# Kernel tuning notes

Measured on AMD Instinct MI355X. Metric: run time of the kernel, lower is better.

The kernel has to match this reference:

```python
import jax, jax.numpy as jnp
import numpy as np

D_MODEL = 128; D_STATE = 64; D_CONV = 4; EXPAND = 2; HEADDIM = 32; NGROUPS = 1
D_INNER = EXPAND * D_MODEL            # 256
NHEADS = D_INNER // HEADDIM           # 8
CONV_DIM = D_INNER + 2 * NGROUPS * D_STATE   # 384 (x, B, C streams)
D_IN_PROJ = 2 * D_INNER + 2 * NGROUPS * D_STATE + NHEADS  # 648 (z, xBC, dt)
EPS = 1e-5


def setup_inputs() -> dict:
    key = jax.random.key(0)
    ks = jax.random.split(key, 8)
    B, L = 8, 4096
    x = jax.random.normal(ks[0], (B, L, D_MODEL), jnp.float32)
    norm_w = jnp.ones((D_MODEL,), jnp.float32)
    in_proj_w = jax.random.normal(ks[1], (D_IN_PROJ, D_MODEL), jnp.float32) * (D_MODEL ** -0.5)
    conv_w = jax.random.normal(ks[2], (CONV_DIM, D_CONV), jnp.float32) * (D_CONV ** -0.5)
    conv_b = jnp.zeros((CONV_DIM,), jnp.float32)
    dt_bias = jax.random.uniform(ks[3], (NHEADS,), jnp.float32, -4.0, -1.0)
    A_log = jnp.log(jax.random.uniform(ks[4], (NHEADS,), jnp.float32, 1.0, 16.0))
    D = jnp.ones((NHEADS,), jnp.float32)
    gnorm_w = jnp.ones((D_INNER,), jnp.float32)
    out_proj_w = jax.random.normal(ks[5], (D_MODEL, D_INNER), jnp.float32) * (D_INNER ** -0.5)
    return dict(x=x, norm_w=norm_w, in_proj_w=in_proj_w, conv_w=conv_w, conv_b=conv_b,
                dt_bias=dt_bias, A_log=A_log, D=D, gnorm_w=gnorm_w, out_proj_w=out_proj_w)


def _rmsnorm(x, w):
    return x * jax.lax.rsqrt(jnp.mean(x * x, axis=-1, keepdims=True) + EPS) * w


def _causal_dw_conv(x, w, b):
    # x: [B,L,C]; w: [C,K]; depthwise causal conv along L
    K = w.shape[1]
    xp = jnp.pad(x, ((0, 0), (K - 1, 0), (0, 0)))
    kern = jnp.transpose(w)[:, None, :]  # [K,1,C] for WIO with groups=C
    out = jax.lax.conv_general_dilated(
        xp, kern, window_strides=(1,), padding='VALID',
        dimension_numbers=('NWC', 'WIO', 'NWC'),
        feature_group_count=w.shape[0])
    return out + b


def _ssm(xh, dt, Bm, Cm, A):
    # xh: [B,L,H,P]; dt: [B,L,H]; Bm, Cm: [B,L,N]; A: [H]
    def step(h, inp):
        x_t, dt_t, B_t, C_t = inp
        dA = jnp.exp(dt_t * A)                                   # [B,H]
        h = h * dA[..., None, None] + (dt_t[..., None] * x_t)[..., None] * B_t[:, None, None, :]
        y = jnp.einsum('bhpn,bn->bhp', h, C_t)
        return h, y
    Bsz, L, H, P = xh.shape
    N = Bm.shape[-1]
    h0 = jnp.zeros((Bsz, H, P, N), xh.dtype)
    xs = (xh.transpose(1, 0, 2, 3), dt.transpose(1, 0, 2),
          Bm.transpose(1, 0, 2), Cm.transpose(1, 0, 2))
    _, ys = jax.lax.scan(step, h0, xs)
    return ys.transpose(1, 0, 2, 3)  # [B,L,H,P]


def reference(x, norm_w, in_proj_w, conv_w, conv_b, dt_bias, A_log, D, gnorm_w, out_proj_w):
    xn = _rmsnorm(x, norm_w)
    zxbcdt = xn @ in_proj_w.T                                    # [B,L,648]
    z, xBC, dt = jnp.split(zxbcdt, [D_INNER, D_INNER + CONV_DIM], axis=-1)
    dt = jax.nn.softplus(dt + dt_bias)                           # [B,L,H]
    xBC = jax.nn.silu(_causal_dw_conv(xBC, conv_w, conv_b))
    xs, Bm, Cm = jnp.split(xBC, [D_INNER, D_INNER + NGROUPS * D_STATE], axis=-1)
    Bsz, L, _ = x.shape
    xh = xs.reshape(Bsz, L, NHEADS, HEADDIM)
    A = -jnp.exp(A_log)                                          # [H]
    y = _ssm(xh, dt, Bm, Cm, A) + D[None, None, :, None] * xh    # D skip per head
    y = y.reshape(Bsz, L, D_INNER)
    y = _rmsnorm(y * jax.nn.silu(z), gnorm_w)                    # gated RMSNorm
    out = y @ out_proj_w.T
    return x + out
```

## Files before the change

### kernel.cpp

```cpp
#include <hip/hip_runtime.h>

#define DM    128
#define DI    256
#define NH    8
#define HD    32
#define NS    64
#define CDIM  384
#define DPROJ 648
#define LSEQ  4096
#define NB    8
#define NTOK  32768
#define LC    64
#define NC    64
#define EPSF  1e-5f
#define LOG2E 1.4426950408889634f

typedef __bf16 bf16;
typedef bf16  bf16x8 __attribute__((ext_vector_type(8)));
typedef bf16  bf16x4 __attribute__((ext_vector_type(4)));
typedef short short8 __attribute__((ext_vector_type(8)));
typedef float f32x4  __attribute__((ext_vector_type(4)));

__device__ __forceinline__ unsigned short f2bfbits(float f) {
    unsigned int u = __float_as_uint(f);
    unsigned int r = u + 0x7FFFu + ((u >> 16) & 1u);
    return (unsigned short)(r >> 16);
}
__device__ __forceinline__ float bfbits2f(unsigned short u) {
    return __uint_as_float(((unsigned int)u) << 16);
}

__global__ __launch_bounds__(256) void k_prep(const float* __restrict__ w1,
                                              const float* __restrict__ w2,
                                              const float* __restrict__ gw,
                                              unsigned short* __restrict__ w1g,
                                              unsigned short* __restrict__ w2f) {
    int i = blockIdx.x * 256 + threadIdx.x;
    if (i < 640 * DM) {
        int f = i >> 9, r = i & 511;
        int lane = r >> 3, jj = r & 7;
        int ns = f >> 2, kk = f & 3;
        int n = ns * 16 + (lane & 15), k = kk * 32 + (lane >> 4) * 8 + jj;
        w1g[i] = f2bfbits(w1[(size_t)n * DM + k]);
    } else {
        int j = i - 640 * DM;
        if (j < DM * DI) {
            int f = j >> 9, r = j & 511;
            int lane = r >> 3, jj = r & 7;
            int kk = f >> 3, nt = f & 7;
            int fr = lane & 15, ko = lane >> 4;
            int n = nt * 16 + fr, k = kk * 32 + ko * 8 + jj;
            w2f[j] = f2bfbits(w2[(size_t)n * DI + k] * gw[k]);
        }
    }
}

__global__ __launch_bounds__(256, 4) void k_gemm1(const float* __restrict__ x,
                                                  const float* __restrict__ nw,
                                                  const float* __restrict__ w1,
                                                  const float* __restrict__ dtb,
                                                  const unsigned short* __restrict__ w1g,
                                                  unsigned short* __restrict__ zb,
                                                  unsigned short* __restrict__ xbc,
                                                  float* __restrict__ dtf) {
    __shared__ float Xs[64][132];
    __shared__ float Wd[8][132];
    const int t = threadIdx.x;
    const int wave = t >> 6, lane = t & 63;
    const int m0 = blockIdx.x * 64;
    const int ny = blockIdx.y;
    if (ny == 0) {
        int row = t >> 5, col = (t & 31) * 4;
        *(float4*)&Wd[row][col] = *(const float4*)(w1 + (size_t)(640 + row) * DM + col);
    }
    const float nw0 = nw[lane * 2], nw1 = nw[lane * 2 + 1];
    #pragma unroll
    for (int i = 0; i < 16; i++) {
        int r = wave * 16 + i;
        const float* xr = x + (size_t)(m0 + r) * DM + lane * 2;
        float v0 = xr[0], v1 = xr[1];
        float ss = v0 * v0 + v1 * v1;
        #pragma unroll
        for (int o = 32; o; o >>= 1) ss += __shfl_xor(ss, o);
        float rs = rsqrtf(ss * (1.0f / DM) + EPSF);
        Xs[r][lane * 2]     = v0 * rs * nw0;
        Xs[r][lane * 2 + 1] = v1 * rs * nw1;
    }
    __syncthreads();
    if (ny == 0) {
        const int h = lane >> 3, ks = lane & 7;
        const float dtbh = dtb[h];
        #pragma unroll
        for (int i = 0; i < 16; i++) {
            int r = wave * 16 + i;
            float acc = 0.f;
            #pragma unroll
            for (int q = 0; q < 4; q++) {
                float4 xv = *(const float4*)&Xs[r][ks * 16 + q * 4];
                float4 wv = *(const float4*)&Wd[h][ks * 16 + q * 4];
                acc = fmaf(xv.x, wv.x, acc); acc = fmaf(xv.y, wv.y, acc);
                acc = fmaf(xv.z, wv.z, acc); acc = fmaf(xv.w, wv.w, acc);
            }
            acc += __shfl_xor(acc, 1);
            acc += __shfl_xor(acc, 2);
            acc += __shfl_xor(acc, 4);
            if (ks == 0) {
                float v = acc + dtbh;
                dtf[(size_t)(m0 + r) * NH + h] = (v > 20.f) ? v : log1pf(expf(v));
            }
        }
    }
    const int wm = wave >> 1, wn = wave & 1;
    const int fr = lane & 15, ko = lane >> 4;
    bf16x8 a[2][4];
    #pragma unroll
    for (int mt = 0; mt < 2; mt++)
        #pragma unroll
        for (int kk = 0; kk < 4; kk++) {
            const float* src = &Xs[wm * 32 + mt * 16 + fr][kk * 32 + ko * 8];
            float4 lo = *(const float4*)src, hi = *(const float4*)(src + 4);
            bf16x8 af;
            af[0] = (bf16)lo.x; af[1] = (bf16)lo.y; af[2] = (bf16)lo.z; af[3] = (bf16)lo.w;
            af[4] = (bf16)hi.x; af[5] = (bf16)hi.y; af[6] = (bf16)hi.z; af[7] = (bf16)hi.w;
            a[mt][kk] = af;
        }
    for (int i = 0; i < 5; i++) {
        int nt = ny * 5 + i;
        const unsigned short* wb = w1g + (((size_t)(nt * 4 + wn * 2) * 4) << 9) + lane * 8;
        f32x4 acc[2][2] = {};
        #pragma unroll
        for (int kk = 0; kk < 4; kk++) {
            bf16x8 b0 = *(const bf16x8*)(wb + ((size_t)kk << 9));
            bf16x8 b1 = *(const bf16x8*)(wb + ((size_t)(4 + kk) << 9));
            acc[0][0] = __builtin_amdgcn_mfma_f32_16x16x32_bf16(a[0][kk], b0, acc[0][0], 0, 0, 0);
            acc[1][0] = __builtin_amdgcn_mfma_f32_16x16x32_bf16(a[1][kk], b0, acc[1][0], 0, 0, 0);
            acc[0][1] = __builtin_amdgcn_mfma_f32_16x16x32_bf16(a[0][kk], b1, acc[0][1], 0, 0, 0);
            acc[1][1] = __builtin_amdgcn_mfma_f32_16x16x32_bf16(a[1][kk], b1, acc[1][1], 0, 0, 0);
        }
        unsigned short* dst; int ld, nc0;
        if (nt < 4) { dst = zb;  ld = DI;   nc0 = nt * 64; }
        else        { dst = xbc; ld = CDIM; nc0 = nt * 64 - 256; }
        #pragma unroll
        for (int mt = 0; mt < 2; mt++)
            #pragma unroll
            for (int ntt = 0; ntt < 2; ntt++) {
                int n = nc0 + wn * 32 + ntt * 16 + fr;
                #pragma unroll
                for (int rr = 0; rr < 4; rr++) {
                    int m = m0 + wm * 32 + mt * 16 + ko * 4 + rr;
                    dst[(size_t)m * ld + n] = f2bfbits(acc[mt][ntt][rr]);
                }
            }
    }
}

__global__ __launch_bounds__(512) void k_conv1(const unsigned short* __restrict__ xbc,
                                               const float* __restrict__ cw,
                                               const float* __restrict__ cb,
                                               const float* __restrict__ dtf,
                                               const float* __restrict__ alog,
                                               unsigned short* __restrict__ bcA,
                                               unsigned short* __restrict__ xT,
                                               unsigned short* __restrict__ hst,
                                               float* __restrict__ dAp) {
    __shared__ __align__(16) unsigned short L[320][72];
    __shared__ float wlh[NH][64];
    const int tid = threadIdx.x;
    const int t0 = blockIdx.x * 64;
    if (tid < CDIM) {
        const int ch = tid;
        const int l0 = t0 & (LSEQ - 1);
        float4 wv = *(const float4*)(cw + ch * 4);
        float bias = cb[ch];
        const unsigned short* in = xbc + (size_t)t0 * CDIM + ch;
        float h1 = 0.f, h2 = 0.f, h3 = 0.f;
        if (l0) {
            h1 = bfbits2f(in[-CDIM]);
            h2 = bfbits2f(in[-2 * CDIM]);
            h3 = bfbits2f(in[-3 * CDIM]);
        }
        short8 pk;
        #pragma unroll 8
        for (int t = 0; t < 64; t++) {
            float x0 = bfbits2f(in[(size_t)t * CDIM]);
            float acc = bias;
            acc = fmaf(x0, wv.w, acc);
            acc = fmaf(h1, wv.z, acc);
            acc = fmaf(h2, wv.y, acc);
            acc = fmaf(h3, wv.x, acc);
            float s = acc / (1.f + expf(-acc));
            unsigned short us = f2bfbits(s);
            if (ch >= 256) bcA[(size_t)(t0 + t) * 128 + (ch - 256)] = us;
            pk[t & 7] = (short)us;
            if (ch < 320 && (t & 7) == 7) *(short8*)&L[ch][t - 7] = pk;
            h3 = h2; h2 = h1; h1 = x0;
        }
    }
    __syncthreads();
    {
        int idx = tid;
        #pragma unroll
        for (int it = 0; it < 4; it++, idx += 512) {
            int row = idx >> 3, tc = (idx & 7) * 8;
            *(short8*)(xT + (size_t)row * NTOK + t0 + tc) = *(const short8*)&L[row][tc];
        }
    }
    const int h = tid >> 6, lane = tid & 63;
    const int b = blockIdx.x >> 6, c = blockIdx.x & 63;
    const int bh = b * NH + h;
    const float A = -expf(alog[h]);
    float dt = dtf[(size_t)(t0 + lane) * NH + h];
    float q = dt * A * LOG2E;
    #pragma unroll
    for (int o = 1; o <= 32; o <<= 1) {
        float tmp = __shfl_up(q, o);
        if (lane >= o) q += tmp;
    }
    float qL = __shfl(q, 63);
    wlh[h][lane] = exp2f(qL - q) * dt;
    if (lane == 0) dAp[(size_t)bh * NC + c] = exp2f(qL);
    const int m = lane & 15, ko = lane >> 4;
    f32x4 hacc[4][2] = {};
    #pragma unroll
    for (int kh = 0; kh < 2; kh++) {
        bf16x8 xb[2];
        #pragma unroll
        for (int pi = 0; pi < 2; pi++)
            xb[pi] = *(const bf16x8*)&L[h * HD + pi * 16 + m][kh * 32 + ko * 8];
        f32x4 w0 = *(const f32x4*)&wlh[h][kh * 32 + ko * 8];
        f32x4 w1v = *(const f32x4*)&wlh[h][kh * 32 + ko * 8 + 4];
        #pragma unroll
        for (int ni = 0; ni < 4; ni++) {
            bf16x8 bv = *(const bf16x8*)&L[256 + ni * 16 + m][kh * 32 + ko * 8];
            bf16x8 af;
            #pragma unroll
            for (int j = 0; j < 4; j++) af[j] = (bf16)((float)bv[j] * w0[j]);
            #pragma unroll
            for (int j = 0; j < 4; j++) af[4 + j] = (bf16)((float)bv[4 + j] * w1v[j]);
            #pragma unroll
            for (int pi = 0; pi < 2; pi++)
                hacc[ni][pi] = __builtin_amdgcn_mfma_f32_16x16x32_bf16(af, xb[pi], hacc[ni][pi], 0, 0, 0);
        }
    }
    unsigned short* hb = hst + (((size_t)bh * NC + c) << 11);
    #pragma unroll
    for (int ni = 0; ni < 4; ni++)
        #pragma unroll
        for (int pi = 0; pi < 2; pi++) {
            bf16x4 pv;
            #pragma unroll
            for (int r = 0; r < 4; r++) pv[r] = (bf16)hacc[ni][pi][r];
            *(bf16x4*)(hb + (pi * 16 + m) * 64 + ni * 16 + ko * 4) = pv;
        }
}

__global__ __launch_bounds__(256) void k_ssm2(unsigned short* __restrict__ hst,
                                              const float* __restrict__ dAp) {
    __shared__ float dl[NC];
    const int bh = blockIdx.x >> 3, seg = blockIdx.x & 7;
    const int s = seg * 256 + threadIdx.x;
    if (threadIdx.x < NC) dl[threadIdx.x] = dAp[(size_t)bh * NC + threadIdx.x];
    __syncthreads();
    unsigned short* p = hst + ((size_t)bh * NC << 11) + s;
    float r = 0.f;
    float v0 = bfbits2f(p[0]);
    float v1 = bfbits2f(p[(size_t)1 << 11]);
    float v2 = bfbits2f(p[(size_t)2 << 11]);
    float v3 = bfbits2f(p[(size_t)3 << 11]);
    for (int c = 0; c < NC; c += 4) {
        float t;
        t = v0; if (c + 4 < NC) v0 = bfbits2f(p[(size_t)(c + 4) << 11]);
        p[(size_t)c << 11] = f2bfbits(r);       r = fmaf(r, dl[c], t);
        t = v1; if (c + 5 < NC) v1 = bfbits2f(p[(size_t)(c + 5) << 11]);
        p[(size_t)(c + 1) << 11] = f2bfbits(r); r = fmaf(r, dl[c + 1], t);
        t = v2; if (c + 6 < NC) v2 = bfbits2f(p[(size_t)(c + 6) << 11]);
        p[(size_t)(c + 2) << 11] = f2bfbits(r); r = fmaf(r, dl[c + 2], t);
        t = v3; if (c + 7 < NC) v3 = bfbits2f(p[(size_t)(c + 7) << 11]);
        p[(size_t)(c + 3) << 11] = f2bfbits(r); r = fmaf(r, dl[c + 3], t);
    }
}

__global__ __launch_bounds__(512, 2) void k_ssd3g(const unsigned short* __restrict__ bcA,
                                                  const unsigned short* __restrict__ xT,
                                                  const float* __restrict__ dtf,
                                                  const float* __restrict__ alog,
                                                  const unsigned short* __restrict__ hst,
                                                  const float* __restrict__ Dw,
                                                  const unsigned short* __restrict__ zb,
                                                  const unsigned short* __restrict__ w2f,
                                                  const float* __restrict__ xin,
                                                  float* __restrict__ out) {
    __shared__ __align__(16) unsigned short BC[64][136];
    __shared__ __align__(16) bf16 PlY[NH][64 * 40];
    __shared__ float ql[NH][64];
    __shared__ float dl[NH][64];
    const int tid = threadIdx.x;
    const int b = blockIdx.x >> 6, c = blockIdx.x & 63;
    const int t0 = blockIdx.x * 64;
    const size_t tok0 = (size_t)t0;
    {
        int idx = tid;
        #pragma unroll
        for (int it = 0; it < 2; it++, idx += 512) {
            int tok = idx >> 4, c8 = (idx & 15) * 8;
            *(short8*)&BC[tok][c8] = *(const short8*)(bcA + (tok0 + tok) * 128 + c8);
        }
    }
    __syncthreads();
    const int h = tid >> 6, lane = tid & 63;
    const int bh = b * NH + h;
    const float A = -expf(alog[h]);
    const float Dh = Dw[h];
    float dt = dtf[(tok0 + lane) * NH + h];
    float q = dt * A * LOG2E;
    #pragma unroll
    for (int o = 1; o <= 32; o <<= 1) {
        float tmp = __shfl_up(q, o);
        if (lane >= o) q += tmp;
    }
    ql[h][lane] = q;
    dl[h][lane] = dt;
    const int m = lane & 15, ko = lane >> 4;
    bf16* Pw = &PlY[h][0];
    bf16x8 cf[4][2];
    #pragma unroll
    for (int ti = 0; ti < 4; ti++)
        #pragma unroll
        for (int kh = 0; kh < 2; kh++)
            cf[ti][kh] = *(const bf16x8*)&BC[ti * 16 + m][64 + kh * 32 + ko * 8];
    float qt[4];
    #pragma unroll
    for (int ti = 0; ti < 4; ti++) qt[ti] = ql[h][ti * 16 + m];
    const size_t hbase = ((size_t)bh * NC + c) << 11;
    f32x4 ya[4][2] = {}, ua[4][2] = {};
    #pragma unroll
    for (int kh = 0; kh < 2; kh++) {
        bf16x8 hb2[2];
        #pragma unroll
        for (int pi = 0; pi < 2; pi++)
            hb2[pi] = *(const bf16x8*)(hst + hbase + (pi * 16 + m) * 64 + kh * 32 + ko * 8);
        #pragma unroll
        for (int ti = 0; ti < 4; ti++)
            #pragma unroll
            for (int pi = 0; pi < 2; pi++)
                ua[ti][pi] = __builtin_amdgcn_mfma_f32_16x16x32_bf16(cf[ti][kh], hb2[pi], ua[ti][pi], 0, 0, 0);
    }
    #pragma unroll
    for (int sh = 0; sh < 2; sh++) {
        f32x4 gth[4][2] = {};
        #pragma unroll
        for (int kh = 0; kh < 2; kh++) {
            bf16x8 bfg[2];
            #pragma unroll
            for (int sj = 0; sj < 2; sj++)
                bfg[sj] = *(const bf16x8*)&BC[(sh * 2 + sj) * 16 + m][kh * 32 + ko * 8];
            #pragma unroll
            for (int ti = 0; ti < 4; ti++)
                #pragma unroll
                for (int sj = 0; sj < 2; sj++)
                    gth[ti][sj] = __builtin_amdgcn_mfma_f32_16x16x32_bf16(bfg[sj], cf[ti][kh], gth[ti][sj], 0, 0, 0);
        }
        #pragma unroll
        for (int sj = 0; sj < 2; sj++) {
            const int si = sh * 2 + sj;
            f32x4 qs = *(const f32x4*)&ql[h][si * 16 + ko * 4];
            f32x4 ds = *(const f32x4*)&dl[h][si * 16 + ko * 4];
            #pragma unroll
            for (int ti = 0; ti < 4; ti++) {
                bf16x4 pv = {};
                if (si <= ti) {
                    const int t = ti * 16 + m;
                    #pragma unroll
                    for (int r = 0; r < 4; r++) {
                        int s = si * 16 + ko * 4 + r;
                        float p = 0.f;
                        if (s <= t) {
                            p = exp2f(qt[ti] - qs[r]) * ds[r] * gth[ti][sj][r];
                            if (s == t) p += Dh;
                        }
                        pv[r] = (bf16)p;
                    }
                }
                *(bf16x4*)&Pw[(ti * 16 + m) * 40 + sj * 16 + ko * 4] = pv;
            }
        }
        bf16x8 xb[2];
        #pragma unroll
        for (int pi = 0; pi < 2; pi++)
            xb[pi] = *(const bf16x8*)(xT + (size_t)(h * HD + pi * 16 + m) * NTOK + tok0 + sh * 32 + ko * 8);
        #pragma unroll
        for (int ti = 0; ti < 4; ti++) {
            bf16x8 pa = *(const bf16x8*)&Pw[(ti * 16 + m) * 40 + ko * 8];
            #pragma unroll
            for (int pi = 0; pi < 2; pi++)
                ya[ti][pi] = __builtin_amdgcn_mfma_f32_16x16x32_bf16(pa, xb[pi], ya[ti][pi], 0, 0, 0);
        }
    }
    __syncthreads();
    unsigned short* Ys = (unsigned short*)&PlY[0][0];
    {
        f32x4 et[4];
        #pragma unroll
        for (int ti = 0; ti < 4; ti++) {
            f32x4 qv = *(const f32x4*)&ql[h][ti * 16 + ko * 4];
            #pragma unroll
            for (int r = 0; r < 4; r++) et[ti][r] = exp2f(qv[r]);
        }
        #pragma unroll
        for (int ti = 0; ti < 4; ti++)
            #pragma unroll
            for (int pi = 0; pi < 2; pi++)
                #pragma unroll
                for (int r = 0; r < 4; r++) {
                    int t = ti * 16 + ko * 4 + r;
                    Ys[t * 264 + h * HD + pi * 16 + m] =
                        f2bfbits(ya[ti][pi][r] + et[ti][r] * ua[ti][pi][r]);
                }
    }
    __syncthreads();
    {
        const int rg = h & 3, nh = h >> 2;
        const int r0 = rg * 16;
        const size_t rowo = (tok0 + r0 + m) * DI;
        float ss = 0.f;
        bf16x8 gb[8];
        #pragma unroll
        for (int kk = 0; kk < 8; kk++) {
            int co = kk * 32 + ko * 8;
            bf16x8 yv = *(const bf16x8*)&Ys[(r0 + m) * 264 + co];
            bf16x8 zv = *(const bf16x8*)(zb + rowo + co);
            #pragma unroll
            for (int j = 0; j < 8; j++) {
                float z = (float)zv[j];
                float g = (float)yv[j] * (z / (1.f + expf(-z)));
                ss += g * g;
                gb[kk][j] = (bf16)g;
            }
        }
        ss += __shfl_xor(ss, 16);
        ss += __shfl_xor(ss, 32);
        const float rs = rsqrtf(ss * (1.0f / DI) + EPSF);
        #pragma unroll
        for (int kk = 0; kk < 8; kk++)
            #pragma unroll
            for (int j = 0; j < 8; j++)
                gb[kk][j] = (bf16)((float)gb[kk][j] * rs);
        const unsigned short* wp = w2f + (size_t)lane * 8;
        f32x4 acc[4] = {};
        #pragma unroll
        for (int kk = 0; kk < 8; kk++) {
            #pragma unroll
            for (int ntl = 0; ntl < 4; ntl++) {
                bf16x8 bfr = *(const bf16x8*)(wp + (((size_t)kk * 8 + nh * 4 + ntl) << 9));
                acc[ntl] = __builtin_amdgcn_mfma_f32_16x16x32_bf16(gb[kk], bfr, acc[ntl], 0, 0, 0);
            }
        }
        #pragma unroll
        for (int ntl = 0; ntl < 4; ntl++) {
            int n = (nh * 4 + ntl) * 16 + m;
            #pragma unroll
            for (int rr = 0; rr < 4; rr++) {
                size_t row = tok0 + r0 + ko * 4 + rr;
                out[row * DM + n] = xin[row * DM + n] + acc[ntl][rr];
            }
        }
    }
}

extern "C" void kernel_launch(void* const* d_in, const int* in_sizes, int n_in,
                              void* d_out, int out_size, void* d_ws, size_t ws_size,
                              hipStream_t stream) {
    const float* x   = (const float*)d_in[0];
    const float* nw  = (const float*)d_in[1];
    const float* w1  = (const float*)d_in[2];
    const float* cw  = (const float*)d_in[3];
    const float* cb  = (const float*)d_in[4];
    const float* dtb = (const float*)d_in[5];
    const float* al  = (const float*)d_in[6];
    const float* Dw  = (const float*)d_in[7];
    const float* gw  = (const float*)d_in[8];
    const float* w2  = (const float*)d_in[9];
    float* out = (float*)d_out;

    float* ws = (float*)d_ws;
    float*  dAp = ws;
    float*  dtf = dAp + NB * NH * NC;
    unsigned short* hst = (unsigned short*)(dtf + (size_t)NTOK * NH);
    unsigned short* zb  = hst + (size_t)NB * NH * NC * 2048;
    unsigned short* xbc = zb + (size_t)NTOK * DI;
    unsigned short* bcA = xbc + (size_t)NTOK * CDIM;
    unsigned short* xT  = bcA + (size_t)NTOK * 128;
    unsigned short* w1g = xT + (size_t)DI * NTOK;
    unsigned short* w2f = w1g + (size_t)640 * DM;

    k_prep<<<(640 * DM + DM * DI + 255) / 256, 256, 0, stream>>>(w1, w2, gw, w1g, w2f);
    k_gemm1<<<dim3(NTOK / 64, 2), 256, 0, stream>>>(x, nw, w1, dtb, w1g, zb, xbc, dtf);
    k_conv1<<<NTOK / 64, 512, 0, stream>>>(xbc, cw, cb, dtf, al, bcA, xT, hst, dAp);
    k_ssm2<<<NB * NH * 8, 256, 0, stream>>>(hst, dAp);
    k_ssd3g<<<NTOK / 64, 512, 0, stream>>>(bcA, xT, dtf, al, hst, Dw, zb, w2f, x, out);
}
```

Measured before the change: 177.0 us.

## Fuse input projection GEMM with causal conv and chunk-state computation

```diff
diff --git a/kernel.cpp b/kernel.cpp
--- a/kernel.cpp
+++ b/kernel.cpp
@@ -55,49 +55,62 @@
     }
 }
 
-__global__ __launch_bounds__(256, 4) void k_gemm1(const float* __restrict__ x,
-                                                  const float* __restrict__ nw,
-                                                  const float* __restrict__ w1,
-                                                  const float* __restrict__ dtb,
-                                                  const unsigned short* __restrict__ w1g,
-                                                  unsigned short* __restrict__ zb,
-                                                  unsigned short* __restrict__ xbc,
-                                                  float* __restrict__ dtf) {
-    __shared__ float Xs[64][132];
-    __shared__ float Wd[8][132];
-    const int t = threadIdx.x;
-    const int wave = t >> 6, lane = t & 63;
-    const int m0 = blockIdx.x * 64;
-    const int ny = blockIdx.y;
-    if (ny == 0) {
-        int row = t >> 5, col = (t & 31) * 4;
-        *(float4*)&Wd[row][col] = *(const float4*)(w1 + (size_t)(640 + row) * DM + col);
+__global__ __launch_bounds__(512) void k_front(const float* __restrict__ x,
+                                               const float* __restrict__ nw,
+                                               const float* __restrict__ w1,
+                                               const float* __restrict__ dtb,
+                                               const unsigned short* __restrict__ w1g,
+                                               const float* __restrict__ cw,
+                                               const float* __restrict__ cb,
+                                               const float* __restrict__ alog,
+                                               unsigned short* __restrict__ zb,
+                                               float* __restrict__ dtf,
+                                               unsigned short* __restrict__ bcA,
+                                               unsigned short* __restrict__ xT,
+                                               unsigned short* __restrict__ hst,
+                                               float* __restrict__ dAp) {
+    __shared__ __align__(16) unsigned char SMEM[117120];
+    unsigned short* XBC = (unsigned short*)SMEM;
+    float*          Xs  = (float*)(SMEM + 62720);
+    unsigned short* Lc  = (unsigned short*)(SMEM + 62720);
+    float*          Wd  = (float*)(SMEM + 108800);
+    float*          dts = (float*)(SMEM + 113024);
+    float*          wlh = (float*)(SMEM + 115072);
+    const int tid = threadIdx.x;
+    const int wave = tid >> 6, lane = tid & 63;
+    const int t0 = blockIdx.x * 64;
+    const int l0 = t0 & (LSEQ - 1);
+    if (tid < 256) {
+        int row = tid >> 5, col = (tid & 31) * 4;
+        *(float4*)&Wd[row * 132 + col] = *(const float4*)(w1 + (size_t)(640 + row) * DM + col);
     }
     const float nw0 = nw[lane * 2], nw1 = nw[lane * 2 + 1];
     #pragma unroll
-    for (int i = 0; i < 16; i++) {
-        int r = wave * 16 + i;
-        const float* xr = x + (size_t)(m0 + r) * DM + lane * 2;
+    for (int i = 0; i < 10; i++) {
+        int r = wave * 10 + i;
+        int tok = t0 + r - 16; if (tok < 0) tok = 0;
+        const float* xr = x + (size_t)tok * DM + lane * 2;
         float v0 = xr[0], v1 = xr[1];
         float ss = v0 * v0 + v1 * v1;
         #pragma unroll
         for (int o = 32; o; o >>= 1) ss += __shfl_xor(ss, o);
         float rs = rsqrtf(ss * (1.0f / DM) + EPSF);
-        Xs[r][lane * 2]     = v0 * rs * nw0;
-        Xs[r][lane * 2 + 1] = v1 * rs * nw1;
-    }
-    __syncthreads();
-    if (ny == 0) {
+        Xs[r * 132 + lane * 2]     = v0 * rs * nw0;
+        Xs[r * 132 + lane * 2 + 1] = v1 * rs * nw1;
+    }
+    __syncthreads();
+    {
         const int h = lane >> 3, ks = lane & 7;
         const float dtbh = dtb[h];
         #pragma unroll
-        for (int i = 0; i < 16; i++) {
-            int r = wave * 16 + i;
+        for (int i = 0; i < 8; i++) {
+            int rw = wave * 8 + i;
+            int r = 16 + rw;
             float acc = 0.f;
             #pragma unroll
             for (int q = 0; q < 4; q++) {
-                float4 xv = *(const float4*)&Xs[r][ks * 16 + q * 4];
-                float4 wv = *(const float4*)&Wd[h][ks * 16 + q * 4];
+                float4 xv = *(const float4*)&Xs[r * 132 + ks * 16 + q * 4];
+                float4 wv = *(const float4*)&Wd[h * 132 + ks * 16 + q * 4];
                 acc = fmaf(xv.x, wv.x, acc); acc = fmaf(xv.y, wv.y, acc);
                 acc = fmaf(xv.z, wv.z, acc); acc = fmaf(xv.w, wv.w, acc);
             }
@@ -106,83 +119,75 @@
             acc += __shfl_xor(acc, 4);
             if (ks == 0) {
                 float v = acc + dtbh;
-                dtf[(size_t)(m0 + r) * NH + h] = (v > 20.f) ? v : log1pf(expf(v));
-            }
-        }
-    }
-    const int wm = wave >> 1, wn = wave & 1;
+                float sp = (v > 20.f) ? v : log1pf(expf(v));
+                dtf[(size_t)(t0 + rw) * NH + h] = sp;
+                dts[rw * NH + h] = sp;
+            }
+        }
+    }
+    const int wm = wave >> 2, wn = wave & 3;
     const int fr = lane & 15, ko = lane >> 4;
-    bf16x8 a[2][4];
-    #pragma unroll
-    for (int mt = 0; mt < 2; mt++)
+    bf16x8 a0[4], a1[4], ah[4];
+    #pragma unroll
+    for (int kk = 0; kk < 4; kk++) {
+        const float* s0 = &Xs[(16 + wm * 32 + fr) * 132 + kk * 32 + ko * 8];
+        const float* s1 = &Xs[(16 + wm * 32 + 16 + fr) * 132 + kk * 32 + ko * 8];
+        const float* sh = &Xs[fr * 132 + kk * 32 + ko * 8];
+        bf16x8 f0, f1, fh;
+        #pragma unroll
+        for (int j = 0; j < 8; j++) {
+            f0[j] = (bf16)s0[j]; f1[j] = (bf16)s1[j]; fh[j] = (bf16)sh[j];
+        }
+        a0[kk] = f0; a1[kk] = f1; ah[kk] = fh;
+    }
+    for (int i = 0; i < 10; i++) {
+        int f = i * 4 + wn;
+        const unsigned short* wb = w1g + (((size_t)f * 4) << 9) + lane * 8;
+        f32x4 acc0 = {}, acc1 = {}, accH = {};
         #pragma unroll
         for (int kk = 0; kk < 4; kk++) {
-            const float* src = &Xs[wm * 32 + mt * 16 + fr][kk * 32 + ko * 8];
-            float4 lo = *(const float4*)src, hi = *(const float4*)(src + 4);
-            bf16x8 af;
-            af[0] = (bf16)lo.x; af[1] = (bf16)lo.y; af[2] = (bf16)lo.z; af[3] = (bf16)lo.w;
-            af[4] = (bf16)hi.x; af[5] = (bf16)hi.y; af[6] = (bf16)hi.z; af[7] = (bf16)hi.w;
-            a[mt][kk] = af;
-        }
-    for (int i = 0; i < 5; i++) {
-        int nt = ny * 5 + i;
-        const unsigned short* wb = w1g + (((size_t)(nt * 4 + wn * 2) * 4) << 9) + lane * 8;
-        f32x4 acc[2][2] = {};
-        #pragma unroll
-        for (int kk = 0; kk < 4; kk++) {
-            bf16x8 b0 = *(const bf16x8*)(wb + ((size_t)kk << 9));
-            bf16x8 b1 = *(const bf16x8*)(wb + ((size_t)(4 + kk) << 9));
-            acc[0][0] = __builtin_amdgcn_mfma_f32_16x16x32_bf16(a[0][kk], b0, acc[0][0], 0, 0, 0);
-            acc[1][0] = __builtin_amdgcn_mfma_f32_16x16x32_bf16(a[1][kk], b0, acc[1][0], 0, 0, 0);
-            acc[0][1] = __builtin_amdgcn_mfma_f32_16x16x32_bf16(a[0][kk], b1, acc[0][1], 0, 0, 0);
-            acc[1][1] = __builtin_amdgcn_mfma_f32_16x16x32_bf16(a[1][kk], b1, acc[1][1], 0, 0, 0);
-        }
-        unsigned short* dst; int ld, nc0;
-        if (nt < 4) { dst = zb;  ld = DI;   nc0 = nt * 64; }
-        else        { dst = xbc; ld = CDIM; nc0 = nt * 64 - 256; }
-        #pragma unroll
-        for (int mt = 0; mt < 2; mt++)
-            #pragma unroll
-            for (int ntt = 0; ntt < 2; ntt++) {
-                int n = nc0 + wn * 32 + ntt * 16 + fr;
-                #pragma unroll
-                for (int rr = 0; rr < 4; rr++) {
-                    int m = m0 + wm * 32 + mt * 16 + ko * 4 + rr;
-                    dst[(size_t)m * ld + n] = f2bfbits(acc[mt][ntt][rr]);
-                }
-            }
-    }
-}
-
-__global__ __launch_bounds__(512) void k_conv1(const unsigned short* __restrict__ xbc,
-                                               const float* __restrict__ cw,
-                                               const float* __restrict__ cb,
-                                               const float* __restrict__ dtf,
-                                               const float* __restrict__ alog,
-                                               unsigned short* __restrict__ bcA,
-                                               unsigned short* __restrict__ xT,
-                                               unsigned short* __restrict__ hst,
-                                               float* __restrict__ dAp) {
-    __shared__ __align__(16) unsigned short L[320][72];
-    __shared__ float wlh[NH][64];
-    const int tid = threadIdx.x;
-    const int t0 = blockIdx.x * 64;
+            bf16x8 bfr = *(const bf16x8*)(wb + ((size_t)kk << 9));
+            acc0 = __builtin_amdgcn_mfma_f32_16x16x32_bf16(a0[kk], bfr, acc0, 0, 0, 0);
+            acc1 = __builtin_amdgcn_mfma_f32_16x16x32_bf16(a1[kk], bfr, acc1, 0, 0, 0);
+            if (i >= 4 && wm == 0)
+                accH = __builtin_amdgcn_mfma_f32_16x16x32_bf16(ah[kk], bfr, accH, 0, 0, 0);
+        }
+        if (i < 4) {
+            int n = f * 16 + fr;
+            #pragma unroll
+            for (int rr = 0; rr < 4; rr++) {
+                zb[(size_t)(t0 + wm * 32 + ko * 4 + rr) * DI + n]      = f2bfbits(acc0[rr]);
+                zb[(size_t)(t0 + wm * 32 + 16 + ko * 4 + rr) * DI + n] = f2bfbits(acc1[rr]);
+            }
+        } else {
+            int cc = f * 16 + fr - 256;
+            #pragma unroll
+            for (int rr = 0; rr < 4; rr++) {
+                XBC[(16 + wm * 32 + ko * 4 + rr) * 392 + cc]      = f2bfbits(acc0[rr]);
+                XBC[(16 + wm * 32 + 16 + ko * 4 + rr) * 392 + cc] = f2bfbits(acc1[rr]);
+            }
+            if (wm == 0) {
+                #pragma unroll
+                for (int rr = 0; rr < 4; rr++)
+                    XBC[(ko * 4 + rr) * 392 + cc] = f2bfbits(accH[rr]);
+            }
+        }
+    }
+    __syncthreads();
     if (tid < CDIM) {
         const int ch = tid;
-        const int l0 = t0 & (LSEQ - 1);
         float4 wv = *(const float4*)(cw + ch * 4);
         float bias = cb[ch];
-        const unsigned short* in = xbc + (size_t)t0 * CDIM + ch;
         float h1 = 0.f, h2 = 0.f, h3 = 0.f;
         if (l0) {
-            h1 = bfbits2f(in[-CDIM]);
-            h2 = bfbits2f(in[-2 * CDIM]);
-            h3 = bfbits2f(in[-3 * CDIM]);
+            h1 = bfbits2f(XBC[15 * 392 + ch]);
+            h2 = bfbits2f(XBC[14 * 392 + ch]);
+            h3 = bfbits2f(XBC[13 * 392 + ch]);
         }
         short8 pk;
         #pragma unroll 8
         for (int t = 0; t < 64; t++) {
-            float x0 = bfbits2f(in[(size_t)t * CDIM]);
+            float x0 = bfbits2f(XBC[(16 + t) * 392 + ch]);
             float acc = bias;
             acc = fmaf(x0, wv.w, acc);
             acc = fmaf(h1, wv.z, acc);
@@ -192,7 +197,7 @@
             unsigned short us = f2bfbits(s);
             if (ch >= 256) bcA[(size_t)(t0 + t) * 128 + (ch - 256)] = us;
             pk[t & 7] = (short)us;
-            if (ch < 320 && (t & 7) == 7) *(short8*)&L[ch][t - 7] = pk;
+            if (ch < 320 && (t & 7) == 7) *(short8*)&Lc[ch * 72 + t - 7] = pk;
             h3 = h2; h2 = h1; h1 = x0;
         }
     }
@@ -202,56 +207,58 @@
         #pragma unroll
         for (int it = 0; it < 4; it++, idx += 512) {
             int row = idx >> 3, tc = (idx & 7) * 8;
-            *(short8*)(xT + (size_t)row * NTOK + t0 + tc) = *(const short8*)&L[row][tc];
-        }
-    }
-    const int h = tid >> 6, lane = tid & 63;
-    const int b = blockIdx.x >> 6, c = blockIdx.x & 63;
-    const int bh = b * NH + h;
-    const float A = -expf(alog[h]);
-    float dt = dtf[(size_t)(t0 + lane) * NH + h];
-    float q = dt * A * LOG2E;
-    #pragma unroll
-    for (int o = 1; o <= 32; o <<= 1) {
-        float tmp = __shfl_up(q, o);
-        if (lane >= o) q += tmp;
-    }
-    float qL = __shfl(q, 63);
-    wlh[h][lane] = exp2f(qL - q) * dt;
-    if (lane == 0) dAp[(size_t)bh * NC + c] = exp2f(qL);
-    const int m = lane & 15, ko = lane >> 4;
-    f32x4 hacc[4][2] = {};
-    #pragma unroll
-    for (int kh = 0; kh < 2; kh++) {
-        bf16x8 xb[2];
-        #pragma unroll
-        for (int pi = 0; pi < 2; pi++)
-            xb[pi] = *(const bf16x8*)&L[h * HD + pi * 16 + m][kh * 32 + ko * 8];
-        f32x4 w0 = *(const f32x4*)&wlh[h][kh * 32 + ko * 8];
-        f32x4 w1v = *(const f32x4*)&wlh[h][kh * 32 + ko * 8 + 4];
-        #pragma unroll
-        for (int ni = 0; ni < 4; ni++) {
-            bf16x8 bv = *(const bf16x8*)&L[256 + ni * 16 + m][kh * 32 + ko * 8];
-            bf16x8 af;
-            #pragma unroll
-            for (int j = 0; j < 4; j++) af[j] = (bf16)((float)bv[j] * w0[j]);
-            #pragma unroll
-            for (int j = 0; j < 4; j++) af[4 + j] = (bf16)((float)bv[4 + j] * w1v[j]);
+            *(short8*)(xT + (size_t)row * NTOK + t0 + tc) = *(const short8*)&Lc[row * 72 + tc];
+        }
+    }
+    {
+        const int h = wave;
+        const int b = blockIdx.x >> 6, c = blockIdx.x & 63;
+        const int bh = b * NH + h;
+        const float A = -expf(alog[h]);
+        float dt = dts[lane * NH + h];
+        float q = dt * A * LOG2E;
+        #pragma unroll
+        for (int o = 1; o <= 32; o <<= 1) {
+            float tmp = __shfl_up(q, o);
+            if (lane >= o) q += tmp;
+        }
+        float qL = __shfl(q, 63);
+        wlh[h * 64 + lane] = exp2f(qL - q) * dt;
+        if (lane == 0) dAp[(size_t)bh * NC + c] = exp2f(qL);
+        const int m = lane & 15;
+        f32x4 hacc[4][2] = {};
+        #pragma unroll
+        for (int kh = 0; kh < 2; kh++) {
+            bf16x8 xb[2];
             #pragma unroll
             for (int pi = 0; pi < 2; pi++)
-                hacc[ni][pi] = __builtin_amdgcn_mfma_f32_16x16x32_bf16(af, xb[pi], hacc[ni][pi], 0, 0, 0);
-        }
-    }
-    unsigned short* hb = hst + (((size_t)bh * NC + c) << 11);
-    #pragma unroll
-    for (int ni = 0; ni < 4; ni++)
-        #pragma unroll
-        for (int pi = 0; pi < 2; pi++) {
-            bf16x4 pv;
-            #pragma unroll
-            for (int r = 0; r < 4; r++) pv[r] = (bf16)hacc[ni][pi][r];
-            *(bf16x4*)(hb + (pi * 16 + m) * 64 + ni * 16 + ko * 4) = pv;
-        }
+                xb[pi] = *(const bf16x8*)&Lc[(h * HD + pi * 16 + m) * 72 + kh * 32 + ko * 8];
+            f32x4 w0 = *(const f32x4*)&wlh[h * 64 + kh * 32 + ko * 8];
+            f32x4 w1v = *(const f32x4*)&wlh[h * 64 + kh * 32 + ko * 8 + 4];
+            #pragma unroll
+            for (int ni = 0; ni < 4; ni++) {
+                bf16x8 bv = *(const bf16x8*)&Lc[(256 + ni * 16 + m) * 72 + kh * 32 + ko * 8];
+                bf16x8 af;
+                #pragma unroll
+                for (int j = 0; j < 4; j++) af[j] = (bf16)((float)bv[j] * w0[j]);
+                #pragma unroll
+                for (int j = 0; j < 4; j++) af[4 + j] = (bf16)((float)bv[4 + j] * w1v[j]);
+                #pragma unroll
+                for (int pi = 0; pi < 2; pi++)
+                    hacc[ni][pi] = __builtin_amdgcn_mfma_f32_16x16x32_bf16(af, xb[pi], hacc[ni][pi], 0, 0, 0);
+            }
+        }
+        unsigned short* hb = hst + (((size_t)bh * NC + c) << 11);
+        #pragma unroll
+        for (int ni = 0; ni < 4; ni++)
+            #pragma unroll
+            for (int pi = 0; pi < 2; pi++) {
+                bf16x4 pv;
+                #pragma unroll
+                for (int r = 0; r < 4; r++) pv[r] = (bf16)hacc[ni][pi][r];
+                *(bf16x4*)(hb + (pi * 16 + m) * 64 + ni * 16 + ko * 4) = pv;
+            }
+    }
 }
 
 __global__ __launch_bounds__(256) void k_ssm2(unsigned short* __restrict__ hst,
@@ -487,15 +494,14 @@
     float*  dtf = dAp + NB * NH * NC;
     unsigned short* hst = (unsigned short*)(dtf + (size_t)NTOK * NH);
     unsigned short* zb  = hst + (size_t)NB * NH * NC * 2048;
-    unsigned short* xbc = zb + (size_t)NTOK * DI;
-    unsigned short* bcA = xbc + (size_t)NTOK * CDIM;
+    unsigned short* bcA = zb + (size_t)NTOK * DI;
     unsigned short* xT  = bcA + (size_t)NTOK * 128;
     unsigned short* w1g = xT + (size_t)DI * NTOK;
     unsigned short* w2f = w1g + (size_t)640 * DM;
 
     k_prep<<<(640 * DM + DM * DI + 255) / 256, 256, 0, stream>>>(w1, w2, gw, w1g, w2f);
-    k_gemm1<<<dim3(NTOK / 64, 2), 256, 0, stream>>>(x, nw, w1, dtb, w1g, zb, xbc, dtf);
-    k_conv1<<<NTOK / 64, 512, 0, stream>>>(xbc, cw, cb, dtf, al, bcA, xT, hst, dAp);
+    k_front<<<NTOK / 64, 512, 0, stream>>>(x, nw, w1, dtb, w1g, cw, cb, al,
+                                           zb, dtf, bcA, xT, hst, dAp);
     k_ssm2<<<NB * NH * 8, 256, 0, stream>>>(hst, dAp);
     k_ssd3g<<<NTOK / 64, 512, 0, stream>>>(bcA, xT, dtf, al, hst, Dw, zb, w2f, x, out);
 }
```

Result: no change. 180.2 us (+1.8%).
